# Performance work log

Measured on AMD Instinct MI355X. Metric: run time of the kernel, lower is better.

The kernel has to match this reference:

```python
import jax, jax.numpy as jnp
import numpy as np

EPS = 1e-5

def conv2d(x, w, b, groups=1):
    out = jax.lax.conv_general_dilated(
        x, w, (1, 1), 'SAME',
        dimension_numbers=('NCHW', 'OIHW', 'NCHW'),
        feature_group_count=groups)
    return out + b[None, :, None, None]

def bilinear_gather(img, ys, xs):
    # img [B,C,H,W]; ys,xs [B,K,H,W] float sample coords; zero padding outside
    H, W = img.shape[2], img.shape[3]
    y0 = jnp.floor(ys)
    x0 = jnp.floor(xs)
    wy = ys - y0
    wx = xs - x0

    def corner(yi, xi, w):
        valid = (yi >= 0) & (yi <= H - 1) & (xi >= 0) & (xi <= W - 1)
        yc = jnp.clip(yi, 0, H - 1).astype(jnp.int32)
        xc = jnp.clip(xi, 0, W - 1).astype(jnp.int32)
        # gather -> [B,C,K,H,W]
        v = jax.vmap(lambda im, y, x: im[:, y, x])(img, yc, xc)
        return v * (w * valid)[:, None]

    return (corner(y0, x0, (1 - wy) * (1 - wx))
            + corner(y0, x0 + 1, (1 - wy) * wx)
            + corner(y0 + 1, x0, wy * (1 - wx))
            + corner(y0 + 1, x0 + 1, wy * wx))

def deform_conv(x, offset, w, b):
    # torchvision DeformConv2d, kernel 3x3, stride 1, pad 1; offset layout [B,2*K,H,W] as (dy,dx) per tap
    B, C, H, W = x.shape
    K = 9
    ky = (jnp.repeat(jnp.arange(3), 3) - 1).astype(x.dtype)  # [9]
    kx = (jnp.tile(jnp.arange(3), 3) - 1).astype(x.dtype)
    off = offset.reshape(B, K, 2, H, W)
    base_y = jnp.arange(H, dtype=x.dtype)[None, None, :, None]
    base_x = jnp.arange(W, dtype=x.dtype)[None, None, None, :]
    ys = base_y + ky[None, :, None, None] + off[:, :, 0]  # [B,K,H,W]
    xs = base_x + kx[None, :, None, None] + off[:, :, 1]
    sampled = bilinear_gather(x, ys, xs)                  # [B,C,K,H,W]
    out = jnp.einsum('bckhw,ock->bohw', sampled, w.reshape(w.shape[0], C, K))
    return out + b[None, :, None, None]

def setup_inputs() -> dict:
    key = jax.random.key(0)
    ks = jax.random.split(key, 12)
    C, O = 128, 128
    B, H, W = 4, 96, 96
    s = 0.05
    return {
        'x': jax.random.normal(ks[0], (B, C, H, W), jnp.float32),
        'dw_w': jax.random.normal(ks[1], (C, 1, 3, 3), jnp.float32) * s,
        'dw_b': jax.random.normal(ks[2], (C,), jnp.float32) * s,
        'pw_w': jax.random.normal(ks[3], (O, C, 1, 1), jnp.float32) * s,
        'pw_b': jax.random.normal(ks[4], (O,), jnp.float32) * s,
        'off_w': jax.random.normal(ks[5], (18, O, 3, 3), jnp.float32) * s,
        'off_b': jax.random.normal(ks[6], (18,), jnp.float32) * s,
        'dc_w': jax.random.normal(ks[7], (O, O, 3, 3), jnp.float32) * s,
        'dc_b': jax.random.normal(ks[8], (O,), jnp.float32) * s,
        'ln_g': jnp.ones((O,), jnp.float32),
        'ln_b': jnp.zeros((O,), jnp.float32),
    }

def reference(x, dw_w, dw_b, pw_w, pw_b, off_w, off_b, dc_w, dc_b, ln_g, ln_b):
    C = x.shape[1]
    # depthwise-separable conv
    h = conv2d(x, dw_w, dw_b, groups=C)
    h = conv2d(h, pw_w, pw_b)
    # InstanceNorm2d (affine=False)
    mu = h.mean((2, 3), keepdims=True)
    var = h.var((2, 3), keepdims=True)
    dsc = (h - mu) * jax.lax.rsqrt(var + EPS)
    # Dropout2d: inference mode -> identity
    offset = conv2d(dsc, off_w, off_b)              # [B,18,H,W]
    dc = deform_conv(dsc, offset, dc_w, dc_b)       # [B,O,H,W]
    # LayerNorm over channels (NHWC last axis)
    nhwc = dc.transpose(0, 2, 3, 1)
    m = nhwc.mean(-1, keepdims=True)
    v = nhwc.var(-1, keepdims=True)
    ln = (nhwc - m) * jax.lax.rsqrt(v + EPS) * ln_g + ln_b
    attn = jax.nn.sigmoid(ln.transpose(0, 3, 1, 2))
    return dsc * attn
```

## Files before the change

### kernel.cpp

```cpp
#include <hip/hip_runtime.h>
#include <math.h>

#define HW 9216
#define WD 96
#define NC 128

typedef unsigned short u16;
typedef __attribute__((ext_vector_type(8))) short short8;
typedef __attribute__((ext_vector_type(4))) float v4f;

__device__ __forceinline__ int rfl(int v){ return __builtin_amdgcn_readfirstlane(v); }
__device__ __forceinline__ float bu2f(u16 s){ return __uint_as_float(((unsigned)s)<<16); }
__device__ __forceinline__ u16 f2b(float f){ unsigned u = __float_as_uint(f);
  return (u16)((u + 0x7fffu + ((u>>16)&1u))>>16); }

__global__ __launch_bounds__(256) void prep_weights(const float* __restrict__ pw_w,
    const float* __restrict__ off_w, const float* __restrict__ dc_w,
    u16* __restrict__ wpwb, u16* __restrict__ wob, u16* __restrict__ wdcb){
  int t = blockIdx.x*256 + threadIdx.x;
  if (t < 16384) wpwb[t] = f2b(pw_w[t]);
  if (t < 36864){
    int ntl = t/18432, rem = t - ntl*18432;
    int s = rem>>9, l = (rem>>3)&63, e = rem&7;
    int o = ntl*16 + (l&15);
    int c = (s&3)*32 + ((l>>4)<<3) + e;
    int k = s>>2;
    wob[t] = (o<18) ? f2b(off_w[(o*128+c)*9+k]) : (u16)0;
  }
  if (t < 147456){
    int e = t&7, l = (t>>3)&63, f = (t>>9)&7, g = t>>12;
    int s = g%18, r = g/18;
    int nt = f>>1, ks = f&1;
    int c = ((s&1)<<6) + ks*32 + ((l>>4)<<3) + e;
    int o = (r<<6) + nt*16 + (l&15);
    int k = s>>1;
    wdcb[t] = f2b(dc_w[(o*128+c)*9 + k]);
  }
}

__global__ __launch_bounds__(256) void dw_conv(const float* __restrict__ x,
    const float* __restrict__ w, const float* __restrict__ bias, u16* __restrict__ h1b){
  int n = blockIdx.x*256 + threadIdx.x;
  int bc = rfl(n / 2304);
  int qp = n - bc*2304;
  int p = qp*4;
  int c = bc & 127;
  int yy = p / WD, xx = p - yy*WD;
  const float* xc = x + (size_t)bc*HW;
  const float* wc = w + c*9;
  float bs = bias[c];
  float a0=bs, a1=bs, a2=bs, a3=bs;
  #pragma unroll
  for (int r=0;r<3;r++){
    int y2 = yy + r - 1;
    if (y2>=0 && y2<96){
      const float* row = xc + y2*WD + xx;
      float4 vc = *(const float4*)row;
      float vl = (xx>0)  ? row[-1] : 0.f;
      float vr = (xx<92) ? row[4]  : 0.f;
      float w0 = wc[r*3+0], w1 = wc[r*3+1], w2 = wc[r*3+2];
      a0 = fmaf(w0, vl,   fmaf(w1, vc.x, fmaf(w2, vc.y, a0)));
      a1 = fmaf(w0, vc.x, fmaf(w1, vc.y, fmaf(w2, vc.z, a1)));
      a2 = fmaf(w0, vc.y, fmaf(w1, vc.z, fmaf(w2, vc.w, a2)));
      a3 = fmaf(w0, vc.z, fmaf(w1, vc.w, fmaf(w2, vr,   a3)));
    }
  }
  ushort4 pk = make_ushort4(f2b(a0), f2b(a1), f2b(a2), f2b(a3));
  *(ushort4*)(h1b + (size_t)bc*HW + p) = pk;
}

__global__ __launch_bounds__(256) void pw_mfma(const u16* __restrict__ h1b,
    const u16* __restrict__ wpwb, const float* __restrict__ pw_b, float* __restrict__ h2){
  __shared__ short Aw[128*136];
  __shared__ short Bw[128*68];
  int blk = blockIdx.x; int row0 = blk*64;
  int b = rfl(row0/HW); int pbase = rfl(row0 - b*HW);
  int t = threadIdx.x;
  #pragma unroll
  for (int i=0;i<8;i++){
    int idx = i*256 + t; int o = idx>>4, seg = idx&15;
    *(short8*)&Aw[o*136 + seg*8] = *(const short8*)(wpwb + o*128 + seg*8);
  }
  #pragma unroll
  for (int i=0;i<4;i++){
    int idx = i*256 + t; int c = idx>>3, seg = idx&7;
    *(short8*)&Bw[c*68 + seg*8] =
      *(const short8*)(h1b + (size_t)(b*NC+c)*HW + pbase + seg*8);
  }
  __syncthreads();
  int w = rfl(t>>6); int l = t&63; int q = l>>4; int ln = l&15;
  v4f acc[8];
  #pragma unroll
  for (int mt=0;mt<8;mt++) acc[mt] = (v4f){0.f,0.f,0.f,0.f};
  #pragma unroll
  for (int ks=0;ks<4;ks++){
    short8 bf;
    #pragma unroll
    for (int j=0;j<8;j++) bf[j] = Bw[(ks*32 + q*8 + j)*68 + w*16 + ln];
    #pragma unroll
    for (int mt=0;mt<8;mt++){
      short8 af = *(short8*)&Aw[(mt*16+ln)*136 + ks*32 + q*8];
      acc[mt] = __builtin_amdgcn_mfma_f32_16x16x32_bf16(af, bf, acc[mt], 0,0,0);
    }
  }
  int px = pbase + w*16 + ln;
  #pragma unroll
  for (int mt=0;mt<8;mt++){
    #pragma unroll
    for (int r=0;r<4;r++){
      int o = mt*16 + q*4 + r;
      h2[(size_t)(b*NC+o)*HW + px] = acc[mt][r] + pw_b[o];
    }
  }
}

__global__ __launch_bounds__(256) void inorm_stats(const float* __restrict__ h2, float* __restrict__ st){
  int bc = blockIdx.x;
  const float4* src = (const float4*)(h2 + (size_t)bc*HW);
  float s=0.f, ss=0.f;
  for (int i=threadIdx.x; i<2304; i+=256){
    float4 v = src[i];
    s += v.x+v.y+v.z+v.w;
    ss = fmaf(v.x,v.x, fmaf(v.y,v.y, fmaf(v.z,v.z, fmaf(v.w,v.w, ss))));
  }
  #pragma unroll
  for (int off=32; off; off>>=1){ s += __shfl_down(s,off); ss += __shfl_down(ss,off); }
  __shared__ float rsm[2][4];
  int wave = threadIdx.x>>6, lane = threadIdx.x&63;
  if (lane==0){ rsm[0][wave]=s; rsm[1][wave]=ss; }
  __syncthreads();
  if (threadIdx.x==0){
    float S = rsm[0][0]+rsm[0][1]+rsm[0][2]+rsm[0][3];
    float SS= rsm[1][0]+rsm[1][1]+rsm[1][2]+rsm[1][3];
    float mu = S * (1.f/9216.f);
    float var = SS * (1.f/9216.f) - mu*mu;
    st[bc*2]   = mu;
    st[bc*2+1] = rsqrtf(var + 1e-5f);
  }
}

__global__ __launch_bounds__(256) void make_dsc(const float* __restrict__ h2,
    const float* __restrict__ st, u16* __restrict__ dscT){
  int blk = blockIdx.x;
  int pt = blk % 144; int r = blk/144; int ch = r & 1; int b = r >> 1;
  int c0 = ch*64, pbase = pt*64;
  __shared__ float tile[64][65];
  int tr = threadIdx.x >> 2;
  int g  = threadIdx.x & 3;
  int c  = c0 + tr;
  float mu = st[(b*128+c)*2];
  float rs = st[(b*128+c)*2+1];
  const float* src = h2 + (size_t)(b*128+c)*HW + pbase + g*16;
  #pragma unroll
  for (int i=0;i<4;i++){
    float4 v = *(const float4*)(src + i*4);
    v.x=(v.x-mu)*rs; v.y=(v.y-mu)*rs; v.z=(v.z-mu)*rs; v.w=(v.w-mu)*rs;
    tile[tr][g*16+i*4+0]=v.x; tile[tr][g*16+i*4+1]=v.y;
    tile[tr][g*16+i*4+2]=v.z; tile[tr][g*16+i*4+3]=v.w;
  }
  __syncthreads();
  int pr = tr;
  u16* dt = dscT + ((size_t)b*HW + pbase + pr)*NC + c0 + g*16;
  #pragma unroll
  for (int i=0;i<4;i++){
    float v0 = tile[g*16+i*4+0][pr], v1 = tile[g*16+i*4+1][pr];
    float v2 = tile[g*16+i*4+2][pr], v3 = tile[g*16+i*4+3][pr];
    ushort4 hi = make_ushort4(f2b(v0), f2b(v1), f2b(v2), f2b(v3));
    *(ushort4*)(dt + i*4) = hi;
  }
}

__global__ __launch_bounds__(256) void off_mfma(const u16* __restrict__ dscT,
    const u16* __restrict__ wobp, const float* __restrict__ off_b,
    float4* __restrict__ wg, ushort4* __restrict__ ad){
  __shared__ short As[2][32*40];
  __shared__ float Po[18*32];
  int blk = blockIdx.x;
  int tile = (blk&7)*144 + (blk>>3);
  int row0 = tile*32;
  int b = rfl(row0/HW); int pbase = rfl(row0 - b*HW);
  int t = threadIdx.x;
  bool stg = t < 128;
  int apx = (t>>2)&31, segA = t&3;
  int w = rfl(t>>6); int l = t&63; int q = l>>4; int ln = l&15;
  int mt = w&1, ntl = w>>1;
  int P = pbase + apx;
  int py = P/96, px_ = P - 96*py;
  const u16* gsrc = dscT + (size_t)b*HW*NC;
  const u16* wbase = wobp + ntl*18432 + l*8;
  uint4 rgA, rgB; short8 bregE, bregO;
  auto issue = [&](int s, uint4& rg){
    int k = s>>2, cseg = s&3;
    int y2 = py + k/3 - 1, x2 = px_ + k%3 - 1;
    bool valid = stg && ((unsigned)y2 < 96u) && ((unsigned)x2 < 96u);
    int off = ((y2*96 + x2)*NC) + cseg*32 + segA*8;
    rg = valid ? *(const uint4*)(gsrc + off) : (uint4){0,0,0,0};
  };
  auto issueB = [&](int s)->short8{
    return *(const short8*)(wbase + s*512);
  };
  auto commit = [&](int buf, uint4& rg){
    if (stg) *(short8*)&As[buf][apx*40 + segA*8] = *(short8*)&rg;
  };
  v4f acc = (v4f){0.f,0.f,0.f,0.f};
  auto step = [&](int buf, short8 bf){
    short8 ah = *(short8*)&As[buf][(mt*16+ln)*40 + q*8];
    acc = __builtin_amdgcn_mfma_f32_16x16x32_bf16(ah, bf, acc, 0,0,0);
  };
  issue(0, rgA); issue(1, rgB);
  bregE = issueB(0); bregO = issueB(1);
  commit(0, rgA);
  __syncthreads();
  #pragma unroll 1
  for (int s=0;s<36;s+=2){
    if (s+2<36) issue(s+2, rgA);
    commit(1, rgB);
    step(0, bregE);
    if (s+2<36) bregE = issueB(s+2);
    __syncthreads();
    if (s+3<36) issue(s+3, rgB);
    if (s+2<36) commit(0, rgA);
    step(1, bregO);
    if (s+3<36) bregO = issueB(s+3);
    __syncthreads();
  }
  int o = ntl*16 + ln;
  if (o < 18){
    float ob = off_b[o];
    #pragma unroll
    for (int r=0;r<4;r++) Po[o*32 + mt*16 + q*4 + r] = acc[r] + ob;
  }
  __syncthreads();
  #pragma unroll
  for (int i=0;i<2;i++){
    int idx = i*256 + t;
    if (idx < 288){
      int pxl = idx & 31, k = idx >> 5;
      int Pp = pbase + pxl;
      float dy = Po[(2*k)*32 + pxl], dx = Po[(2*k+1)*32 + pxl];
      float ys = (float)(Pp/96 + k/3 - 1) + dy;
      float xs = (float)(Pp%96 + k%3 - 1) + dx;
      float fy0 = floorf(ys), fx0 = floorf(xs);
      float wy = ys - fy0, wx = xs - fx0;
      int y0 = (int)fy0, x0 = (int)fx0;
      int y1 = y0+1, x1 = x0+1;
      float vy0 = (y0>=0 && y0<=95) ? 1.f : 0.f;
      float vy1 = (y1>=0 && y1<=95) ? 1.f : 0.f;
      float vx0 = (x0>=0 && x0<=95) ? 1.f : 0.f;
      float vx1 = (x1>=0 && x1<=95) ? 1.f : 0.f;
      int y0c=min(max(y0,0),95), y1c=min(max(y1,0),95);
      int x0c=min(max(x0,0),95), x1c=min(max(x1,0),95);
      float4 w4;
      w4.x = (1.f-wy)*(1.f-wx)*vy0*vx0;
      w4.y = (1.f-wy)*wx*vy0*vx1;
      w4.z = wy*(1.f-wx)*vy1*vx0;
      w4.w = wy*wx*vy1*vx1;
      int gi = (b*9 + k)*HW + pbase + pxl;
      wg[gi] = w4;
      ad[gi] = make_ushort4((u16)(y0c*WD+x0c), (u16)(y0c*WD+x1c),
                            (u16)(y1c*WD+x0c), (u16)(y1c*WD+x1c));
    }
  }
}

__global__ __launch_bounds__(256) void deform_mfma(const u16* __restrict__ dscT,
    const u16* __restrict__ wdcb, const float* __restrict__ dc_b,
    const float4* __restrict__ wg, const ushort4* __restrict__ ad,
    const float* __restrict__ ln_g, const float* __restrict__ ln_b,
    float* __restrict__ out){
  __shared__ short As[2][32*68];
  __shared__ float4 WgL[288];
  __shared__ ushort4 AdL[288];
  __shared__ float RS[2][4][4][4];
  __shared__ u16 DT[32*128];
  int blk = blockIdx.x;
  int tile = (blk&7)*144 + (blk>>3);
  int row0 = tile*32;
  int b = rfl(row0/HW); int pbase = rfl(row0 - b*HW);
  int t = threadIdx.x;
  int apx = t>>3, cs8 = t&7;
  int w = rfl(t>>6); int l = t&63; int q = l>>4; int ln = l&15;
  int mt = w&1, nb = (w>>1)*4, rrole = rfl(w>>1);
  const u16* db0 = dscT + (size_t)b*HW*NC + cs8*8;
  const u16* wbase = wdcb + (size_t)rrole*(18*4096) + l*8;
  #pragma unroll
  for (int i=0;i<2;i++){
    int idx = i*256 + t;
    if (idx < 288){ int k = idx>>5, pxl = idx&31; int gi = (b*9+k)*HW + pbase + pxl;
      WgL[idx] = wg[gi]; AdL[idx] = ad[gi]; }
  }
  __syncthreads();
  uint4 gA0,gA1,gA2,gA3, gB0,gB1,gB2,gB3;
  float4 wvA, wvB;
  short8 bregE[8], bregO[8];
  auto issueG = [&](int s, float4& wv, uint4& r0, uint4& r1, uint4& r2, uint4& r3){
    int k = s>>1, cb = (s&1)<<6;
    ushort4 av = AdL[k*32+apx]; wv = WgL[k*32+apx];
    const u16* db = db0 + cb;
    r0 = *(const uint4*)(db + (int)av.x*NC);
    r1 = *(const uint4*)(db + (int)av.y*NC);
    r2 = *(const uint4*)(db + (int)av.z*NC);
    r3 = *(const uint4*)(db + (int)av.w*NC);
  };
  auto issueB = [&](int s, short8* dst){
    const u16* p = wbase + s*4096;
    #pragma unroll
    for (int f=0;f<8;f++) dst[f] = *(const short8*)(p + f*512);
  };
  auto commitA = [&](int buf, float4 wv, uint4& r0, uint4& r1, uint4& r2, uint4& r3){
    const u16* pa=(const u16*)&r0; const u16* pb=(const u16*)&r1;
    const u16* pc=(const u16*)&r2; const u16* pd=(const u16*)&r3;
    short8 sv;
    #pragma unroll
    for (int j=0;j<8;j++){
      float f = wv.x*bu2f(pa[j]) + wv.y*bu2f(pb[j]) + wv.z*bu2f(pc[j]) + wv.w*bu2f(pd[j]);
      sv[j] = (short)f2b(f);
    }
    *(short8*)&As[buf][apx*68 + cs8*8] = sv;
  };
  v4f acc[4];
  #pragma unroll
  for (int nt=0;nt<4;nt++) acc[nt] = (v4f){0.f,0.f,0.f,0.f};
  auto step = [&](int buf, const short8* bb){
    #pragma unroll
    for (int ks=0;ks<2;ks++){
      short8 af = *(const short8*)&As[buf][(mt*16+ln)*68 + ks*32 + q*8];
      #pragma unroll
      for (int nt=0;nt<4;nt++)
        acc[nt] = __builtin_amdgcn_mfma_f32_16x16x32_bf16(af, bb[nt*2+ks], acc[nt], 0,0,0);
    }
  };
  issueG(0, wvA, gA0,gA1,gA2,gA3); issueB(0, bregE);
  issueG(1, wvB, gB0,gB1,gB2,gB3); issueB(1, bregO);
  commitA(0, wvA, gA0,gA1,gA2,gA3);
  __syncthreads();
  #pragma unroll 1
  for (int s=0;s<18;s+=2){
    if (s+2<18) issueG(s+2, wvA, gA0,gA1,gA2,gA3);
    commitA(1, wvB, gB0,gB1,gB2,gB3);
    step(0, bregE);
    if (s+2<18) issueB(s+2, bregE);
    __syncthreads();
    if (s+3<18) issueG(s+3, wvB, gB0,gB1,gB2,gB3);
    if (s+2<18) commitA(0, wvA, gA0,gA1,gA2,gA3);
    step(1, bregO);
    if (s+3<18) issueB(s+3, bregO);
    __syncthreads();
  }
  int o_[4]; float bias_[4], g_[4], bb_[4];
  #pragma unroll
  for (int nt=0;nt<4;nt++){
    int o = (nb+nt)*16 + ln;
    o_[nt] = o; bias_[nt] = dc_b[o]; g_[nt] = ln_g[o]; bb_[nt] = ln_b[o];
  }
  float s_[4] = {0.f,0.f,0.f,0.f}, ss_[4] = {0.f,0.f,0.f,0.f};
  #pragma unroll
  for (int r=0;r<4;r++){
    #pragma unroll
    for (int nt=0;nt<4;nt++){
      float v = acc[nt][r] + bias_[nt];
      s_[r] += v; ss_[r] = fmaf(v, v, ss_[r]);
    }
  }
  #pragma unroll
  for (int off=1; off<16; off<<=1){
    #pragma unroll
    for (int r=0;r<4;r++){
      s_[r]  += __shfl_xor(s_[r],  off);
      ss_[r] += __shfl_xor(ss_[r], off);
    }
  }
  if (ln==0){
    #pragma unroll
    for (int r=0;r<4;r++){ RS[0][w][q][r] = s_[r]; RS[1][w][q][r] = ss_[r]; }
  }
  {
    const u16* dsrc = dscT + ((size_t)b*HW + pbase)*NC;
    #pragma unroll
    for (int i=0;i<2;i++){
      int idx = i*256 + t;
      *(short8*)&DT[idx*8] = *(const short8*)(dsrc + idx*8);
    }
  }
  __syncthreads();
  float m_[4], rs_[4];
  #pragma unroll
  for (int r=0;r<4;r++){
    float S  = RS[0][w][q][r] + RS[0][w^2][q][r];
    float SS = RS[1][w][q][r] + RS[1][w^2][q][r];
    float m = S*(1.f/128.f);
    float var = SS*(1.f/128.f) - m*m;
    m_[r] = m; rs_[r] = rsqrtf(var + 1e-5f);
  }
  int pxb = pbase + mt*16 + q*4;
  int lpx = mt*16 + q*4;
  #pragma unroll
  for (int nt=0;nt<4;nt++){
    size_t base = (size_t)(b*NC + o_[nt])*HW + pxb;
    float4 ov;
    #pragma unroll
    for (int r=0;r<4;r++){
      float v = acc[nt][r] + bias_[nt];
      float lnv = (v - m_[r])*rs_[r]*g_[nt] + bb_[nt];
      float attn = 1.f/(1.f+__expf(-lnv));
      float dv = bu2f(DT[(lpx+r)*128 + o_[nt]]);
      ((float*)&ov)[r] = dv * attn;
    }
    *(float4*)(out + base) = ov;
  }
}

extern "C" void kernel_launch(void* const* d_in, const int* in_sizes, int n_in,
                              void* d_out, int out_size, void* d_ws, size_t ws_size,
                              hipStream_t stream){
  const float* x    = (const float*)d_in[0];
  const float* dw_w = (const float*)d_in[1];
  const float* dw_b = (const float*)d_in[2];
  const float* pw_w = (const float*)d_in[3];
  const float* pw_b = (const float*)d_in[4];
  const float* off_w= (const float*)d_in[5];
  const float* off_b= (const float*)d_in[6];
  const float* dc_w = (const float*)d_in[7];
  const float* dc_b = (const float*)d_in[8];
  const float* ln_g = (const float*)d_in[9];
  const float* ln_b = (const float*)d_in[10];
  float* out = (float*)d_out;

  float* W    = (float*)d_ws;
  u16*     h1b  = (u16*)W;
  float*   bufB = W + 4718592;
  u16*     dscT = (u16*)(W + 9437184);
  float4*  wg   = (float4*)(W + 14155776);
  ushort4* ad   = (ushort4*)(W + 15482880);
  float*   st   = W + 16146432;
  u16*     wpwb = (u16*)(W + 16147456);
  u16*     wob  = (u16*)(W + 16155648);
  u16*     wdcb = (u16*)(W + 16174080);

  prep_weights<<<576, 256, 0, stream>>>(pw_w, off_w, dc_w, wpwb, wob, wdcb);
  dw_conv     <<<4608, 256, 0, stream>>>(x, dw_w, dw_b, h1b);
  pw_mfma     <<<576, 256, 0, stream>>>(h1b, wpwb, pw_b, bufB);
  inorm_stats <<<512, 256, 0, stream>>>(bufB, st);
  make_dsc    <<<1152, 256, 0, stream>>>(bufB, st, dscT);
  off_mfma    <<<1152, 256, 0, stream>>>(dscT, wob, off_b, wg, ad);
  deform_mfma <<<1152, 256, 0, stream>>>(dscT, wdcb, dc_b, wg, ad, ln_g, ln_b, out);
}
```

Measured before the change: 177.2 us.

## Fuse instance-norm statistics into pointwise GEMM epilogue and store bf16 intermediate

The pointwise MFMA kernel now reduces per-channel sum and sum-of-squares across lanes and waves and adds them atomically into a stats buffer, which prep_weights zeroes. This removes the separate inorm_stats pass that re-read the full fp32 intermediate. The intermediate is also stored as bf16, roughly halving its write and read traffic in make_dsc. In exchange it adds atomics, bf16 rounding before normalization, and the one-pass E[x^2]-mu^2 variance is accumulated across blocks in fp32.

```diff
diff --git a/kernel.cpp b/kernel.cpp
--- a/kernel.cpp
+++ b/kernel.cpp
@@ -16,8 +16,10 @@
 
 __global__ __launch_bounds__(256) void prep_weights(const float* __restrict__ pw_w,
     const float* __restrict__ off_w, const float* __restrict__ dc_w,
-    u16* __restrict__ wpwb, u16* __restrict__ wob, u16* __restrict__ wdcb){
+    u16* __restrict__ wpwb, u16* __restrict__ wob, u16* __restrict__ wdcb,
+    float* __restrict__ st2){
   int t = blockIdx.x*256 + threadIdx.x;
+  if (t < 1024) st2[t] = 0.f;
   if (t < 16384) wpwb[t] = f2b(pw_w[t]);
   if (t < 36864){
     int ntl = t/18432, rem = t - ntl*18432;
@@ -70,9 +72,11 @@
 }
 
 __global__ __launch_bounds__(256) void pw_mfma(const u16* __restrict__ h1b,
-    const u16* __restrict__ wpwb, const float* __restrict__ pw_b, float* __restrict__ h2){
+    const u16* __restrict__ wpwb, const float* __restrict__ pw_b,
+    u16* __restrict__ h2b, float* __restrict__ st2){
   __shared__ short Aw[128*136];
   __shared__ short Bw[128*68];
+  __shared__ float PS[4][128], PSS[4][128];
   int blk = blockIdx.x; int row0 = blk*64;
   int b = rfl(row0/HW); int pbase = rfl(row0 - b*HW);
   int t = threadIdx.x;
@@ -106,41 +110,36 @@
   int px = pbase + w*16 + ln;
   #pragma unroll
   for (int mt=0;mt<8;mt++){
+    float sv[4], ssv[4];
     #pragma unroll
     for (int r=0;r<4;r++){
       int o = mt*16 + q*4 + r;
-      h2[(size_t)(b*NC+o)*HW + px] = acc[mt][r] + pw_b[o];
-    }
-  }
-}
-
-__global__ __launch_bounds__(256) void inorm_stats(const float* __restrict__ h2, float* __restrict__ st){
-  int bc = blockIdx.x;
-  const float4* src = (const float4*)(h2 + (size_t)bc*HW);
-  float s=0.f, ss=0.f;
-  for (int i=threadIdx.x; i<2304; i+=256){
-    float4 v = src[i];
-    s += v.x+v.y+v.z+v.w;
-    ss = fmaf(v.x,v.x, fmaf(v.y,v.y, fmaf(v.z,v.z, fmaf(v.w,v.w, ss))));
-  }
-  #pragma unroll
-  for (int off=32; off; off>>=1){ s += __shfl_down(s,off); ss += __shfl_down(ss,off); }
-  __shared__ float rsm[2][4];
-  int wave = threadIdx.x>>6, lane = threadIdx.x&63;
-  if (lane==0){ rsm[0][wave]=s; rsm[1][wave]=ss; }
-  __syncthreads();
-  if (threadIdx.x==0){
-    float S = rsm[0][0]+rsm[0][1]+rsm[0][2]+rsm[0][3];
-    float SS= rsm[1][0]+rsm[1][1]+rsm[1][2]+rsm[1][3];
-    float mu = S * (1.f/9216.f);
-    float var = SS * (1.f/9216.f) - mu*mu;
-    st[bc*2]   = mu;
-    st[bc*2+1] = rsqrtf(var + 1e-5f);
-  }
-}
-
-__global__ __launch_bounds__(256) void make_dsc(const float* __restrict__ h2,
-    const float* __restrict__ st, u16* __restrict__ dscT){
+      float v = acc[mt][r] + pw_b[o];
+      h2b[(size_t)(b*NC+o)*HW + px] = f2b(v);
+      sv[r] = v; ssv[r] = v*v;
+    }
+    #pragma unroll
+    for (int off=1; off<16; off<<=1){
+      #pragma unroll
+      for (int r=0;r<4;r++){ sv[r] += __shfl_xor(sv[r],off); ssv[r] += __shfl_xor(ssv[r],off); }
+    }
+    if (ln==0){
+      #pragma unroll
+      for (int r=0;r<4;r++){ PS[w][mt*16+q*4+r] = sv[r]; PSS[w][mt*16+q*4+r] = ssv[r]; }
+    }
+  }
+  __syncthreads();
+  if (t < 128){
+    int o = t;
+    float S  = PS[0][o]+PS[1][o]+PS[2][o]+PS[3][o];
+    float SS = PSS[0][o]+PSS[1][o]+PSS[2][o]+PSS[3][o];
+    atomicAdd(&st2[(b*128+o)*2],   S);
+    atomicAdd(&st2[(b*128+o)*2+1], SS);
+  }
+}
+
+__global__ __launch_bounds__(256) void make_dsc(const u16* __restrict__ h2b,
+    const float* __restrict__ st2, u16* __restrict__ dscT){
   int blk = blockIdx.x;
   int pt = blk % 144; int r = blk/144; int ch = r & 1; int b = r >> 1;
   int c0 = ch*64, pbase = pt*64;
@@ -148,15 +147,20 @@
   int tr = threadIdx.x >> 2;
   int g  = threadIdx.x & 3;
   int c  = c0 + tr;
-  float mu = st[(b*128+c)*2];
-  float rs = st[(b*128+c)*2+1];
-  const float* src = h2 + (size_t)(b*128+c)*HW + pbase + g*16;
-  #pragma unroll
-  for (int i=0;i<4;i++){
-    float4 v = *(const float4*)(src + i*4);
-    v.x=(v.x-mu)*rs; v.y=(v.y-mu)*rs; v.z=(v.z-mu)*rs; v.w=(v.w-mu)*rs;
-    tile[tr][g*16+i*4+0]=v.x; tile[tr][g*16+i*4+1]=v.y;
-    tile[tr][g*16+i*4+2]=v.z; tile[tr][g*16+i*4+3]=v.w;
+  float S  = st2[(b*128+c)*2];
+  float SS = st2[(b*128+c)*2+1];
+  float mu = S * (1.f/9216.f);
+  float var = SS * (1.f/9216.f) - mu*mu;
+  float rs = rsqrtf(var + 1e-5f);
+  const u16* src = h2b + (size_t)(b*128+c)*HW + pbase + g*16;
+  #pragma unroll
+  for (int i=0;i<2;i++){
+    short8 v8 = *(const short8*)(src + i*8);
+    #pragma unroll
+    for (int j=0;j<8;j++){
+      float v = (bu2f((u16)v8[j]) - mu)*rs;
+      tile[tr][g*16 + i*8 + j] = v;
+    }
   }
   __syncthreads();
   int pr = tr;
@@ -428,20 +432,19 @@
 
   float* W    = (float*)d_ws;
   u16*     h1b  = (u16*)W;
-  float*   bufB = W + 4718592;
+  u16*     h2b  = (u16*)(W + 4718592);
   u16*     dscT = (u16*)(W + 9437184);
   float4*  wg   = (float4*)(W + 14155776);
   ushort4* ad   = (ushort4*)(W + 15482880);
-  float*   st   = W + 16146432;
+  float*   st2  = W + 16146432;
   u16*     wpwb = (u16*)(W + 16147456);
   u16*     wob  = (u16*)(W + 16155648);
   u16*     wdcb = (u16*)(W + 16174080);
 
-  prep_weights<<<576, 256, 0, stream>>>(pw_w, off_w, dc_w, wpwb, wob, wdcb);
+  prep_weights<<<576, 256, 0, stream>>>(pw_w, off_w, dc_w, wpwb, wob, wdcb, st2);
   dw_conv     <<<4608, 256, 0, stream>>>(x, dw_w, dw_b, h1b);
-  pw_mfma     <<<576, 256, 0, stream>>>(h1b, wpwb, pw_b, bufB);
-  inorm_stats <<<512, 256, 0, stream>>>(bufB, st);
-  make_dsc    <<<1152, 256, 0, stream>>>(bufB, st, dscT);
+  pw_mfma     <<<576, 256, 0, stream>>>(h1b, wpwb, pw_b, h2b, st2);
+  make_dsc    <<<1152, 256, 0, stream>>>(h2b, st2, dscT);
   off_mfma    <<<1152, 256, 0, stream>>>(dscT, wob, off_b, wg, ad);
   deform_mfma <<<1152, 256, 0, stream>>>(dscT, wdcb, dc_b, wg, ad, ln_g, ln_b, out);
 }
```

After: 184.5 us. 1.04x slower.
